# Performance work log

Measured on AMD Instinct MI355X. Metric: run time of the kernel, lower is better.

## Reference

```python
import jax, jax.numpy as jnp
import numpy as np

HEADS = 8
DIM_HEAD = 64
DIM = 512
SCALE = DIM_HEAD ** -0.5
BN_EPS = 1e-5


def setup_inputs() -> dict:
    key = jax.random.key(0)
    ks = jax.random.split(key, 5)
    b, p = 8, 2048
    init = 0.05
    return {
        "x": jax.random.normal(ks[0], (b, p, DIM), jnp.float32),
        "wq": jax.random.normal(ks[1], (HEADS, DIM_HEAD, DIM // HEADS), jnp.float32) * init,
        "wk": jax.random.normal(ks[2], (HEADS, DIM_HEAD, DIM // HEADS), jnp.float32) * init,
        "wv": jax.random.normal(ks[3], (HEADS, DIM_HEAD, DIM // HEADS), jnp.float32) * init,
        "wo": jax.random.normal(ks[4], (DIM, HEADS * DIM_HEAD), jnp.float32) * init,
        "gamma": jnp.ones((DIM,), jnp.float32),
        "beta": jnp.zeros((DIM,), jnp.float32),
    }


def reference(x, wq, wk, wv, wo, gamma, beta):
    # x: [b, p, d]
    b, p, d = x.shape
    h, e = HEADS, DIM_HEAD
    # grouped 1x1 conv == per-head linear on the head's channel slice
    xg = x.reshape(b, p, h, d // h)            # [b, p, h, c]
    q = jnp.einsum('bphc,hec->bhpe', xg, wq)   # [b, h, p, e]
    k = jnp.einsum('bphc,hec->bhpe', xg, wk)
    v = jnp.einsum('bphc,hec->bhpe', xg, wv)
    dots = jnp.einsum('bhie,bhje->bhij', q, k) * SCALE
    attn = jax.nn.softmax(dots, axis=-1)
    out = jnp.einsum('bhij,bhje->bhie', attn, v)     # [b, h, p, e]
    out = out.transpose(0, 2, 1, 3).reshape(b, p, h * e)  # [b, p, inner]
    out = jnp.einsum('bpi,di->bpd', out, wo)         # output 1x1 conv, no bias
    # BatchNorm1d (training mode): stats over (batch, points) per channel
    mean = out.mean(axis=(0, 1))
    var = out.var(axis=(0, 1))
    out = (out - mean) * jax.lax.rsqrt(var + BN_EPS) * gamma + beta
    return jax.nn.relu(out)                          # [b, p, d]
```

## Files before the change

kernel.cpp:

```cpp
#include <hip/hip_runtime.h>
#include <hip/hip_bf16.h>

#define B_ 8
#define P_ 2048
#define D_ 512
#define H_ 8
#define N_ (B_*P_)

using f32x4  = __attribute__((ext_vector_type(4))) float;
using f32x16 = __attribute__((ext_vector_type(16))) float;
using bf16x8 = __attribute__((ext_vector_type(8))) short;

__device__ __forceinline__ unsigned f2bf2(float lo, float hi){
    unsigned short a = __bfloat16_as_ushort(__float2bfloat16(lo));
    unsigned short b = __bfloat16_as_ushort(__float2bfloat16(hi));
    return (unsigned)a | ((unsigned)b << 16);
}
__device__ __forceinline__ unsigned short f2bfu(float x){
    return __bfloat16_as_ushort(__float2bfloat16(x));
}
__device__ __forceinline__ float bf2f(unsigned short u){
    return __uint_as_float(((unsigned)u) << 16);
}
#define SW(r, cb) ((cb) ^ (((r) & 7) << 4))

__device__ __forceinline__ bf16x8 lds_frag(const unsigned char* base, int row, int colb){
    return *(const bf16x8*)(base + row*128 + SW(row, colb));
}

#if __has_builtin(__builtin_amdgcn_exp2f)
#define EXP2(x) __builtin_amdgcn_exp2f(x)
#else
#define EXP2(x) exp2f(x)
#endif

__device__ __forceinline__ void plane32_swap(unsigned &a, unsigned &b){
#if __has_builtin(__builtin_amdgcn_permlane32_swap)
    auto r = __builtin_amdgcn_permlane32_swap(a, b, false, false);
    a = r[0]; b = r[1];
#else
    asm volatile("s_nop 1\n\tv_permlane32_swap_b32 %0, %1\n\ts_nop 1"
                 : "+v"(a), "+v"(b));
#endif
}

#define QSCALE 0.18033688011112042f

__global__ __launch_bounds__(256) void qkv_proj(
        const float* __restrict__ x,
        const float* __restrict__ wq, const float* __restrict__ wk, const float* __restrict__ wv,
        unsigned short* __restrict__ Q, unsigned short* __restrict__ K, unsigned short* __restrict__ Vt)
{
    __shared__ unsigned char xs[128*128];
    __shared__ unsigned char wsh[3][64*128];
    const int t  = threadIdx.x;
    const int bh = blockIdx.x, b = bh >> 3, h = bh & 7;
    const int p0 = blockIdx.y * 128;

    {
        int r = t >> 1, half = t & 1;
        const float4* src = (const float4*)(x + (size_t)(b*P_ + p0 + r)*D_ + h*64 + half*32);
        #pragma unroll
        for (int ci = 0; ci < 4; ci++){
            float4 a = src[ci*2], c = src[ci*2+1];
            uint4 w;
            w.x = f2bf2(a.x, a.y); w.y = f2bf2(a.z, a.w);
            w.z = f2bf2(c.x, c.y); w.w = f2bf2(c.z, c.w);
            *(uint4*)(xs + r*128 + SW(r, half*64 + ci*16)) = w;
        }
    }
    if (t < 192){
        int m = t >> 6, r = t & 63;
        const float* wp = (m == 0 ? wq : (m == 1 ? wk : wv));
        const float4* src = (const float4*)(wp + (size_t)(h*64 + r)*64);
        float sc = (m == 0) ? QSCALE : 1.0f;
        #pragma unroll
        for (int ci = 0; ci < 8; ci++){
            float4 a = src[ci*2], c = src[ci*2+1];
            a.x*=sc;a.y*=sc;a.z*=sc;a.w*=sc; c.x*=sc;c.y*=sc;c.z*=sc;c.w*=sc;
            uint4 w;
            w.x = f2bf2(a.x, a.y); w.y = f2bf2(a.z, a.w);
            w.z = f2bf2(c.x, c.y); w.w = f2bf2(c.z, c.w);
            *(uint4*)(wsh[m] + r*128 + SW(r, ci*16)) = w;
        }
    }
    __syncthreads();
    const int wid = t >> 6, lane = t & 63, g = lane >> 4, l16 = lane & 15;

    bf16x8 fx[2][2];
    #pragma unroll
    for (int pt = 0; pt < 2; pt++)
        #pragma unroll
        for (int kk = 0; kk < 2; kk++)
            fx[pt][kk] = lds_frag(xs, wid*32 + pt*16 + l16, kk*64 + 16*g);

    #pragma unroll
    for (int m = 0; m < 2; m++){
        unsigned short* dst = (m == 0) ? Q : K;
        #pragma unroll
        for (int et = 0; et < 4; et++){
            bf16x8 fw0 = lds_frag(wsh[m], et*16 + l16, 16*g);
            bf16x8 fw1 = lds_frag(wsh[m], et*16 + l16, 64 + 16*g);
            #pragma unroll
            for (int pt = 0; pt < 2; pt++){
                f32x4 acc = {0.f,0.f,0.f,0.f};
                acc = __builtin_amdgcn_mfma_f32_16x16x32_bf16(fw0, fx[pt][0], acc, 0,0,0);
                acc = __builtin_amdgcn_mfma_f32_16x16x32_bf16(fw1, fx[pt][1], acc, 0,0,0);
                int p  = p0 + wid*32 + pt*16 + l16;
                int e0 = et*16 + 4*g;
                uint2 w2; w2.x = f2bf2(acc[0], acc[1]); w2.y = f2bf2(acc[2], acc[3]);
                *(uint2*)(dst + (size_t)(bh*P_ + p)*64 + e0) = w2;
            }
        }
    }
    #pragma unroll
    for (int et = 0; et < 4; et++){
        bf16x8 fw0 = lds_frag(wsh[2], et*16 + l16, 16*g);
        bf16x8 fw1 = lds_frag(wsh[2], et*16 + l16, 64 + 16*g);
        #pragma unroll
        for (int pt = 0; pt < 2; pt++){
            f32x4 acc = {0.f,0.f,0.f,0.f};
            acc = __builtin_amdgcn_mfma_f32_16x16x32_bf16(fx[pt][0], fw0, acc, 0,0,0);
            acc = __builtin_amdgcn_mfma_f32_16x16x32_bf16(fx[pt][1], fw1, acc, 0,0,0);
            int e  = et*16 + l16;
            int pb = p0 + wid*32 + pt*16 + 4*g;
            uint2 w2; w2.x = f2bf2(acc[0], acc[1]); w2.y = f2bf2(acc[2], acc[3]);
            *(uint2*)(Vt + (size_t)(bh*64 + e)*P_ + pb) = w2;
        }
    }
}

__global__ __launch_bounds__(256, 2) void attn_fwd(
        const unsigned short* __restrict__ Q, const unsigned short* __restrict__ K,
        const unsigned short* __restrict__ Vt, unsigned short* __restrict__ AO)
{
    __shared__ unsigned char kshA[64*128], vshA[64*128];
    __shared__ unsigned char kshB[64*128], vshB[64*128];
    const int t  = threadIdx.x;
    const int id = blockIdx.x;
    const int vix = (id & 7) * 128 + (id >> 3);
    const int bh = vix >> 4, b = bh >> 3, h = bh & 7;
    const int q0 = (vix & 15) * 128;
    const int lane = t & 63, wid = t >> 6, hi = lane >> 5, l32 = lane & 31;

    const int qa = q0 + wid*32 + l32;

    bf16x8 fq[4];
    #pragma unroll
    for (int ec = 0; ec < 4; ec++)
        fq[ec] = *(const bf16x8*)(Q + (size_t)(bh*P_ + qa)*64 + ec*16 + hi*8);

    const int srow = t >> 2, sch = t & 3;
    const unsigned short* kgp = K  + ((size_t)bh*P_ + srow)*64 + sch*16;
    const unsigned short* vgp = Vt + ((size_t)(bh*64 + srow))*P_ + sch*16;
    const int wo0 = srow*128 + SW(srow, sch*32);
    const int wo1 = srow*128 + SW(srow, sch*32 + 16);

    f32x16 aco[2];
    #pragma unroll
    for (int r = 0; r < 16; r++){ aco[0][r] = 0.f; aco[1][r] = 0.f; }
    float sml = 0.f;

    uint4 k0, k1, v0, v1;
    auto load_tile = [&](int tt){
        const unsigned short* kp = kgp + (size_t)tt * 4096;
        const unsigned short* vp = vgp + tt * 64;
        k0 = *(const uint4*)kp;        k1 = *(const uint4*)(kp + 8);
        v0 = *(const uint4*)vp;        v1 = *(const uint4*)(vp + 8);
    };
    auto write_tile = [&](unsigned char* ksh, unsigned char* vsh){
        *(uint4*)(ksh + wo0) = k0;  *(uint4*)(ksh + wo1) = k1;
        *(uint4*)(vsh + wo0) = v0;  *(uint4*)(vsh + wo1) = v1;
    };

    auto compute = [&](const unsigned char* ksh, const unsigned char* vsh){
        __builtin_amdgcn_s_setprio(1);
        #pragma unroll
        for (int kb = 0; kb < 2; kb++){
            bf16x8 fk[4], fv[4];
            #pragma unroll
            for (int ec = 0; ec < 4; ec++)
                fk[ec] = *(const bf16x8*)(ksh + (kb*32 + l32)*128 + SW(l32, ec*32 + hi*16));
            #pragma unroll
            for (int sg = 0; sg < 2; sg++)
                #pragma unroll
                for (int eb = 0; eb < 2; eb++)
                    fv[sg*2 + eb] = *(const bf16x8*)(vsh + (eb*32 + l32)*128 + SW(l32, (kb*2 + sg)*32 + hi*16));

            f32x16 s;
            #pragma unroll
            for (int r = 0; r < 16; r++) s[r] = 0.f;
            #pragma unroll
            for (int ec = 0; ec < 4; ec++)
                s = __builtin_amdgcn_mfma_f32_32x32x16_bf16(fk[ec], fq[ec], s, 0, 0, 0);
            float p[16];
            float rs = 0.f;
            #pragma unroll
            for (int r = 0; r < 16; r++){ p[r] = EXP2(s[r]); rs += p[r]; }
            sml += rs;
            #pragma unroll
            for (int sg = 0; sg < 2; sg++){
                unsigned A0 = f2bf2(p[sg*8+0], p[sg*8+1]);
                unsigned A1 = f2bf2(p[sg*8+2], p[sg*8+3]);
                unsigned A2 = f2bf2(p[sg*8+4], p[sg*8+5]);
                unsigned A3 = f2bf2(p[sg*8+6], p[sg*8+7]);
                plane32_swap(A0, A2);
                plane32_swap(A1, A3);
                union { unsigned u[4]; bf16x8 v; } pfu;
                pfu.u[0] = A0; pfu.u[1] = A1; pfu.u[2] = A2; pfu.u[3] = A3;
                #pragma unroll
                for (int eb = 0; eb < 2; eb++)
                    aco[eb] = __builtin_amdgcn_mfma_f32_32x32x16_bf16(fv[sg*2 + eb], pfu.v, aco[eb], 0, 0, 0);
            }
        }
        __builtin_amdgcn_s_setprio(0);
    };

    load_tile(0);
    write_tile(kshA, vshA);
    __syncthreads();

    #pragma unroll 1
    for (int tt = 0; tt < 32; tt += 2){
        load_tile(tt + 1);
        compute(kshA, vshA);
        write_tile(kshB, vshB);
        __syncthreads();
        if (tt + 2 < 32) load_tile(tt + 2);
        compute(kshB, vshB);
        if (tt + 2 < 32){
            write_tile(kshA, vshA);
            __syncthreads();
        }
    }

    float l = sml + __shfl_xor(sml, 32);
    float inv = 1.f / l;
    unsigned short* aor = AO + (size_t)(b*P_ + qa)*D_ + h*64;
    #pragma unroll
    for (int eb = 0; eb < 2; eb++)
        #pragma unroll
        for (int rq = 0; rq < 4; rq++){
            uint2 w;
            w.x = f2bf2(aco[eb][rq*4+0]*inv, aco[eb][rq*4+1]*inv);
            w.y = f2bf2(aco[eb][rq*4+2]*inv, aco[eb][rq*4+3]*inv);
            *(uint2*)(aor + eb*32 + rq*8 + hi*4) = w;
        }
}

__global__ __launch_bounds__(256) void wo_gemm(
        const unsigned short* __restrict__ AO, const float* __restrict__ wo,
        unsigned short* __restrict__ ao2, float* __restrict__ sums)
{
    __shared__ unsigned char ash[128*128];
    __shared__ unsigned char wsh[64*128];
    __shared__ float red[4][2][64];
    const int t  = threadIdx.x;
    const int d0 = blockIdx.x * 64;
    const int n0 = blockIdx.y * 128;
    const int wid = t >> 6, lane = t & 63, g = lane >> 4, l16 = lane & 15;

    f32x4 acc[2][4];
    #pragma unroll
    for (int mt = 0; mt < 2; mt++)
        #pragma unroll
        for (int dt = 0; dt < 4; dt++) acc[mt][dt] = (f32x4){0.f,0.f,0.f,0.f};

    for (int kc = 0; kc < 8; kc++){
        __syncthreads();
        {
            int r = t >> 1, half = t & 1;
            const uint4* src = (const uint4*)(AO + (size_t)(n0 + r)*D_ + kc*64 + half*32);
            #pragma unroll
            for (int i = 0; i < 4; i++)
                *(uint4*)(ash + r*128 + SW(r, half*64 + i*16)) = src[i];
        }
        if (t < 128){
            int r = t >> 1, half = t & 1;
            const float4* src = (const float4*)(wo + (size_t)(d0 + r)*D_ + kc*64 + half*32);
            #pragma unroll
            for (int ci = 0; ci < 4; ci++){
                float4 a = src[ci*2], c = src[ci*2+1];
                uint4 w;
                w.x = f2bf2(a.x, a.y); w.y = f2bf2(a.z, a.w);
                w.z = f2bf2(c.x, c.y); w.w = f2bf2(c.z, c.w);
                *(uint4*)(wsh + r*128 + SW(r, half*64 + ci*16)) = w;
            }
        }
        __syncthreads();
        #pragma unroll
        for (int kk = 0; kk < 2; kk++){
            bf16x8 fa[2], fw[4];
            #pragma unroll
            for (int mt = 0; mt < 2; mt++) fa[mt] = lds_frag(ash, wid*32 + mt*16 + l16, kk*64 + 16*g);
            #pragma unroll
            for (int dt = 0; dt < 4; dt++) fw[dt] = lds_frag(wsh, dt*16 + l16, kk*64 + 16*g);
            #pragma unroll
            for (int mt = 0; mt < 2; mt++)
                #pragma unroll
                for (int dt = 0; dt < 4; dt++)
                    acc[mt][dt] = __builtin_amdgcn_mfma_f32_16x16x32_bf16(fa[mt], fw[dt], acc[mt][dt], 0,0,0);
        }
    }
    float s1[4] = {0.f,0.f,0.f,0.f}, s2[4] = {0.f,0.f,0.f,0.f};
    #pragma unroll
    for (int mt = 0; mt < 2; mt++)
        #pragma unroll
        for (int dt = 0; dt < 4; dt++){
            int d = d0 + dt*16 + l16;
            #pragma unroll
            for (int r = 0; r < 4; r++){
                float v = acc[mt][dt][r];
                ao2[(size_t)(n0 + wid*32 + mt*16 + 4*g + r)*D_ + d] = f2bfu(v);
                s1[dt] += v; s2[dt] += v*v;
            }
        }
    #pragma unroll
    for (int dt = 0; dt < 4; dt++){
        s1[dt] += __shfl_xor(s1[dt], 16); s1[dt] += __shfl_xor(s1[dt], 32);
        s2[dt] += __shfl_xor(s2[dt], 16); s2[dt] += __shfl_xor(s2[dt], 32);
    }
    if (g == 0){
        #pragma unroll
        for (int dt = 0; dt < 4; dt++){
            red[wid][0][dt*16 + l16] = s1[dt];
            red[wid][1][dt*16 + l16] = s2[dt];
        }
    }
    __syncthreads();
    if (t < 128){
        int which = t >> 6, ch = t & 63;
        float v = red[0][which][ch] + red[1][which][ch] + red[2][which][ch] + red[3][which][ch];
        atomicAdd(&sums[which*D_ + d0 + ch], v);
    }
}

__global__ void bn_zero(float* sums){ sums[threadIdx.x] = 0.f; }

__global__ void bn_stats(const float* __restrict__ sums, const float* __restrict__ gamma,
                         const float* __restrict__ beta, float* __restrict__ coef)
{
    int d = threadIdx.x;
    float mean = sums[d] * (1.f/16384.f);
    float var  = sums[512 + d] * (1.f/16384.f) - mean*mean;
    float sc   = gamma[d] * rsqrtf(var + 1e-5f);
    coef[d]       = sc;
    coef[512 + d] = beta[d] - mean*sc;
}

__global__ __launch_bounds__(256) void bn_apply(const unsigned short* __restrict__ ao2,
                                                float* __restrict__ out, const float* __restrict__ coef)
{
    __shared__ float cs[1024];
    int t = threadIdx.x;
    #pragma unroll
    for (int i = 0; i < 4; i++) cs[t + i*256] = coef[t + i*256];
    __syncthreads();
    const int total = N_ * D_ / 8;
    for (int idx = blockIdx.x*256 + t; idx < total; idx += gridDim.x*256){
        uint4 v = *(const uint4*)(ao2 + (size_t)idx*8);
        int d = (idx & 63) * 8;
        float4 o0, o1;
        o0.x = fmaxf(0.f, bf2f((unsigned short)(v.x      ))*cs[d+0] + cs[512+d+0]);
        o0.y = fmaxf(0.f, bf2f((unsigned short)(v.x >> 16))*cs[d+1] + cs[512+d+1]);
        o0.z = fmaxf(0.f, bf2f((unsigned short)(v.y      ))*cs[d+2] + cs[512+d+2]);
        o0.w = fmaxf(0.f, bf2f((unsigned short)(v.y >> 16))*cs[d+3] + cs[512+d+3]);
        o1.x = fmaxf(0.f, bf2f((unsigned short)(v.z      ))*cs[d+4] + cs[512+d+4]);
        o1.y = fmaxf(0.f, bf2f((unsigned short)(v.z >> 16))*cs[d+5] + cs[512+d+5]);
        o1.z = fmaxf(0.f, bf2f((unsigned short)(v.w      ))*cs[d+6] + cs[512+d+6]);
        o1.w = fmaxf(0.f, bf2f((unsigned short)(v.w >> 16))*cs[d+7] + cs[512+d+7]);
        *(float4*)(out + (size_t)idx*8)     = o0;
        *(float4*)(out + (size_t)idx*8 + 4) = o1;
    }
}

extern "C" void kernel_launch(void* const* d_in, const int* in_sizes, int n_in,
                              void* d_out, int out_size, void* d_ws, size_t ws_size,
                              hipStream_t stream)
{
    const float* x     = (const float*)d_in[0];
    const float* wq    = (const float*)d_in[1];
    const float* wk    = (const float*)d_in[2];
    const float* wv    = (const float*)d_in[3];
    const float* wo    = (const float*)d_in[4];
    const float* gamma = (const float*)d_in[5];
    const float* beta  = (const float*)d_in[6];
    float* out = (float*)d_out;

    unsigned char* ws = (unsigned char*)d_ws;
    unsigned short* Q  = (unsigned short*)(ws);
    unsigned short* K  = (unsigned short*)(ws + (16u<<20));
    unsigned short* Vt = (unsigned short*)(ws + (32u<<20));
    unsigned short* AO = (unsigned short*)(ws + (48u<<20));
    float* sums = (float*)(ws + (64u<<20));
    float* coef = sums + 1024;
    unsigned short* AO2 = Q;

    hipLaunchKernelGGL(bn_zero,  dim3(1),       dim3(1024), 0, stream, sums);
    hipLaunchKernelGGL(qkv_proj, dim3(64, 16),  dim3(256),  0, stream, x, wq, wk, wv, Q, K, Vt);
    hipLaunchKernelGGL(attn_fwd, dim3(1024),    dim3(256),  0, stream, Q, K, Vt, AO);
    hipLaunchKernelGGL(wo_gemm,  dim3(8, 128),  dim3(256),  0, stream, AO, wo, AO2, sums);
    hipLaunchKernelGGL(bn_stats, dim3(1),       dim3(512),  0, stream, sums, gamma, beta, coef);
    hipLaunchKernelGGL(bn_apply, dim3(2048),    dim3(256),  0, stream, AO2, out, coef);
}
```

Before: 170.5 us.

## Software-pipeline attention loop: overlap next tile's QK with current tile's softmax+PV

Restructures the flash-attention inner loop so that the QK^T MFMAs for tile t+1 are issued before the exp/pack and PV MFMAs for tile t, carrying V fragments and score accumulators in registers across iterations. The intent is to let the matrix units run while the exponentials and bf16 packing execute, and to hide LDS load latency. In exchange it raises register pressure (extra score accumulators and eight V fragments held live) and adds prologue and epilogue code, which may reduce occupancy.

```diff
diff --git a/kernel.cpp b/kernel.cpp
--- a/kernel.cpp
+++ b/kernel.cpp
@@ -156,9 +156,9 @@
     const int wo0 = srow*128 + SW(srow, sch*32);
     const int wo1 = srow*128 + SW(srow, sch*32 + 16);
 
-    f32x16 aco[2];
-    #pragma unroll
-    for (int r = 0; r < 16; r++){ aco[0][r] = 0.f; aco[1][r] = 0.f; }
+    f32x16 aco0, aco1;
+    #pragma unroll
+    for (int r = 0; r < 16; r++){ aco0[r] = 0.f; aco1[r] = 0.f; }
     float sml = 0.f;
 
     uint4 k0, k1, v0, v1;
@@ -173,30 +173,38 @@
         *(uint4*)(vsh + wo0) = v0;  *(uint4*)(vsh + wo1) = v1;
     };
 
-    auto compute = [&](const unsigned char* ksh, const unsigned char* vsh){
-        __builtin_amdgcn_s_setprio(1);
+    bf16x8 fvc[8];
+    f32x16 sc0, sc1;
+
+    auto qk_tile = [&](const unsigned char* kp_, f32x16& s0, f32x16& s1){
+        bf16x8 fk[8];
+        #pragma unroll
+        for (int kb = 0; kb < 2; kb++)
+            #pragma unroll
+            for (int ec = 0; ec < 4; ec++)
+                fk[kb*4+ec] = *(const bf16x8*)(kp_ + (kb*32 + l32)*128 + SW(l32, ec*32 + hi*16));
+        #pragma unroll
+        for (int r = 0; r < 16; r++){ s0[r] = 0.f; s1[r] = 0.f; }
+        #pragma unroll
+        for (int ec = 0; ec < 4; ec++) s0 = __builtin_amdgcn_mfma_f32_32x32x16_bf16(fk[ec],   fq[ec], s0, 0,0,0);
+        #pragma unroll
+        for (int ec = 0; ec < 4; ec++) s1 = __builtin_amdgcn_mfma_f32_32x32x16_bf16(fk[4+ec], fq[ec], s1, 0,0,0);
+    };
+    auto carry_v = [&](const unsigned char* vp_){
+        #pragma unroll
+        for (int ks = 0; ks < 4; ks++)
+            #pragma unroll
+            for (int eb = 0; eb < 2; eb++)
+                fvc[ks*2+eb] = *(const bf16x8*)(vp_ + (eb*32 + l32)*128 + SW(l32, ks*32 + hi*16));
+    };
+    auto mk_pfu = [&](bf16x8* pfu){
         #pragma unroll
         for (int kb = 0; kb < 2; kb++){
-            bf16x8 fk[4], fv[4];
-            #pragma unroll
-            for (int ec = 0; ec < 4; ec++)
-                fk[ec] = *(const bf16x8*)(ksh + (kb*32 + l32)*128 + SW(l32, ec*32 + hi*16));
-            #pragma unroll
-            for (int sg = 0; sg < 2; sg++)
-                #pragma unroll
-                for (int eb = 0; eb < 2; eb++)
-                    fv[sg*2 + eb] = *(const bf16x8*)(vsh + (eb*32 + l32)*128 + SW(l32, (kb*2 + sg)*32 + hi*16));
-
-            f32x16 s;
-            #pragma unroll
-            for (int r = 0; r < 16; r++) s[r] = 0.f;
-            #pragma unroll
-            for (int ec = 0; ec < 4; ec++)
-                s = __builtin_amdgcn_mfma_f32_32x32x16_bf16(fk[ec], fq[ec], s, 0, 0, 0);
+            const f32x16& sc = kb ? sc1 : sc0;
             float p[16];
             float rs = 0.f;
             #pragma unroll
-            for (int r = 0; r < 16; r++){ p[r] = EXP2(s[r]); rs += p[r]; }
+            for (int r = 0; r < 16; r++){ p[r] = EXP2(sc[r]); rs += p[r]; }
             sml += rs;
             #pragma unroll
             for (int sg = 0; sg < 2; sg++){
@@ -206,46 +214,79 @@
                 unsigned A3 = f2bf2(p[sg*8+6], p[sg*8+7]);
                 plane32_swap(A0, A2);
                 plane32_swap(A1, A3);
-                union { unsigned u[4]; bf16x8 v; } pfu;
-                pfu.u[0] = A0; pfu.u[1] = A1; pfu.u[2] = A2; pfu.u[3] = A3;
-                #pragma unroll
-                for (int eb = 0; eb < 2; eb++)
-                    aco[eb] = __builtin_amdgcn_mfma_f32_32x32x16_bf16(fv[sg*2 + eb], pfu.v, aco[eb], 0, 0, 0);
+                union { unsigned u[4]; bf16x8 v; } pf;
+                pf.u[0]=A0; pf.u[1]=A1; pf.u[2]=A2; pf.u[3]=A3;
+                pfu[kb*2+sg] = pf.v;
             }
         }
-        __builtin_amdgcn_s_setprio(0);
+    };
+    auto pv_tile = [&](const bf16x8* pfu){
+        #pragma unroll
+        for (int ks = 0; ks < 4; ks++){
+            aco0 = __builtin_amdgcn_mfma_f32_32x32x16_bf16(fvc[ks*2+0], pfu[ks], aco0, 0,0,0);
+            aco1 = __builtin_amdgcn_mfma_f32_32x32x16_bf16(fvc[ks*2+1], pfu[ks], aco1, 0,0,0);
+        }
     };
 
     load_tile(0);
     write_tile(kshA, vshA);
     __syncthreads();
+    load_tile(1);
+    qk_tile(kshA, sc0, sc1);
+    carry_v(vshA);
+    write_tile(kshB, vshB);
+    __syncthreads();
+    load_tile(2);
+
+    const unsigned char *kp = kshB, *vp = vshB;
+    unsigned char *kw = kshA, *vw = vshA;
 
     #pragma unroll 1
-    for (int tt = 0; tt < 32; tt += 2){
-        load_tile(tt + 1);
-        compute(kshA, vshA);
-        write_tile(kshB, vshB);
+    for (int tt = 0; tt < 30; ++tt){
+        __builtin_amdgcn_s_setprio(1);
+        f32x16 sn0, sn1;
+        qk_tile(kp, sn0, sn1);
+        bf16x8 pfu[4];
+        mk_pfu(pfu);
+        pv_tile(pfu);
+        __builtin_amdgcn_s_setprio(0);
+        carry_v(vp);
+        sc0 = sn0; sc1 = sn1;
+        write_tile(kw, vw);
         __syncthreads();
-        if (tt + 2 < 32) load_tile(tt + 2);
-        compute(kshB, vshB);
-        if (tt + 2 < 32){
-            write_tile(kshA, vshA);
-            __syncthreads();
-        }
+        if (tt < 29) load_tile(tt + 3);
+        const unsigned char* tk = kp; kp = kw; kw = (unsigned char*)tk;
+        const unsigned char* tv = vp; vp = vw; vw = (unsigned char*)tv;
+    }
+    {
+        f32x16 sn0, sn1;
+        qk_tile(kp, sn0, sn1);
+        bf16x8 pfu[4];
+        mk_pfu(pfu);
+        pv_tile(pfu);
+        carry_v(vp);
+        sc0 = sn0; sc1 = sn1;
+    }
+    {
+        bf16x8 pfu[4];
+        mk_pfu(pfu);
+        pv_tile(pfu);
     }
 
     float l = sml + __shfl_xor(sml, 32);
     float inv = 1.f / l;
     unsigned short* aor = AO + (size_t)(b*P_ + qa)*D_ + h*64;
     #pragma unroll
-    for (int eb = 0; eb < 2; eb++)
+    for (int eb = 0; eb < 2; eb++){
+        const f32x16& a = eb ? aco1 : aco0;
         #pragma unroll
         for (int rq = 0; rq < 4; rq++){
             uint2 w;
-            w.x = f2bf2(aco[eb][rq*4+0]*inv, aco[eb][rq*4+1]*inv);
-            w.y = f2bf2(aco[eb][rq*4+2]*inv, aco[eb][rq*4+3]*inv);
+            w.x = f2bf2(a[rq*4+0]*inv, a[rq*4+1]*inv);
+            w.y = f2bf2(a[rq*4+2]*inv, a[rq*4+3]*inv);
             *(uint2*)(aor + eb*32 + rq*8 + hi*4) = w;
         }
+    }
 }
 
 __global__ __launch_bounds__(256) void wo_gemm(
```

Measured after the change: 174.5 us. +2.3%, slower.

## Store K/V in MFMA fragment order and load fragments directly from global

Applied to the files above, without the earlier changes.

The QKV projection now writes K and V in a pre-swizzled per-tile fragment layout that matches the attention MFMA operand order. The attention kernel then drops its LDS double buffer and block barriers, and each wave reads its K/V fragments straight from global memory with contiguous 16-byte loads. This removes the LDS staging and __syncthreads. In exchange, each of the four waves in a block now fetches the same K/V data from global/L2 on its own instead of sharing it, and the loads are no longer software-pipelined ahead of compute.

```diff
diff --git a/kernel.cpp b/kernel.cpp
--- a/kernel.cpp
+++ b/kernel.cpp
@@ -46,10 +46,17 @@
 
 #define QSCALE 0.18033688011112042f
 
+__device__ __forceinline__ size_t kf_off(int bh, int tt, int kb, int ec, int hi, int l32){
+    return ((size_t)(bh*32 + tt))*4096 + (size_t)(((((kb*4 + ec)*2 + hi)*32) + l32)*8);
+}
+__device__ __forceinline__ size_t vf_off(int bh, int tt, int ks, int eb, int hi, int l32){
+    return ((size_t)(bh*32 + tt))*4096 + (size_t)(((((ks*2 + eb)*2 + hi)*32) + l32)*8);
+}
+
 __global__ __launch_bounds__(256) void qkv_proj(
         const float* __restrict__ x,
         const float* __restrict__ wq, const float* __restrict__ wk, const float* __restrict__ wv,
-        unsigned short* __restrict__ Q, unsigned short* __restrict__ K, unsigned short* __restrict__ Vt)
+        unsigned short* __restrict__ Q, unsigned short* __restrict__ Kf, unsigned short* __restrict__ Vf)
 {
     __shared__ unsigned char xs[128*128];
     __shared__ unsigned char wsh[3][64*128];
@@ -96,7 +103,6 @@
 
     #pragma unroll
     for (int m = 0; m < 2; m++){
-        unsigned short* dst = (m == 0) ? Q : K;
         #pragma unroll
         for (int et = 0; et < 4; et++){
             bf16x8 fw0 = lds_frag(wsh[m], et*16 + l16, 16*g);
@@ -109,7 +115,12 @@
                 int p  = p0 + wid*32 + pt*16 + l16;
                 int e0 = et*16 + 4*g;
                 uint2 w2; w2.x = f2bf2(acc[0], acc[1]); w2.y = f2bf2(acc[2], acc[3]);
-                *(uint2*)(dst + (size_t)(bh*P_ + p)*64 + e0) = w2;
+                if (m == 0){
+                    *(uint2*)(Q + (size_t)(bh*P_ + p)*64 + e0) = w2;
+                } else {
+                    int tt = p >> 6, kvr = p & 63;
+                    *(uint2*)(Kf + kf_off(bh, tt, kvr >> 5, et, g >> 1, kvr & 31) + 4*(g & 1)) = w2;
+                }
             }
         }
     }
@@ -124,18 +135,17 @@
             acc = __builtin_amdgcn_mfma_f32_16x16x32_bf16(fx[pt][1], fw1, acc, 0,0,0);
             int e  = et*16 + l16;
             int pb = p0 + wid*32 + pt*16 + 4*g;
+            int tt = pb >> 6, kvc = pb & 63;
             uint2 w2; w2.x = f2bf2(acc[0], acc[1]); w2.y = f2bf2(acc[2], acc[3]);
-            *(uint2*)(Vt + (size_t)(bh*64 + e)*P_ + pb) = w2;
+            *(uint2*)(Vf + vf_off(bh, tt, kvc >> 4, e >> 5, (kvc >> 3) & 1, e & 31) + (kvc & 7)) = w2;
         }
     }
 }
 
 __global__ __launch_bounds__(256, 2) void attn_fwd(
-        const unsigned short* __restrict__ Q, const unsigned short* __restrict__ K,
-        const unsigned short* __restrict__ Vt, unsigned short* __restrict__ AO)
-{
-    __shared__ unsigned char kshA[64*128], vshA[64*128];
-    __shared__ unsigned char kshB[64*128], vshB[64*128];
+        const unsigned short* __restrict__ Q, const unsigned short* __restrict__ Kf,
+        const unsigned short* __restrict__ Vf, unsigned short* __restrict__ AO)
+{
     const int t  = threadIdx.x;
     const int id = blockIdx.x;
     const int vix = (id & 7) * 128 + (id >> 3);
@@ -150,49 +160,40 @@
     for (int ec = 0; ec < 4; ec++)
         fq[ec] = *(const bf16x8*)(Q + (size_t)(bh*P_ + qa)*64 + ec*16 + hi*8);
 
-    const int srow = t >> 2, sch = t & 3;
-    const unsigned short* kgp = K  + ((size_t)bh*P_ + srow)*64 + sch*16;
-    const unsigned short* vgp = Vt + ((size_t)(bh*64 + srow))*P_ + sch*16;
-    const int wo0 = srow*128 + SW(srow, sch*32);
-    const int wo1 = srow*128 + SW(srow, sch*32 + 16);
+    const unsigned short* kfp = Kf + kf_off(bh, 0, 0, 0, hi, l32);
+    const unsigned short* vfp = Vf + vf_off(bh, 0, 0, 0, hi, l32);
 
     f32x16 aco[2];
     #pragma unroll
     for (int r = 0; r < 16; r++){ aco[0][r] = 0.f; aco[1][r] = 0.f; }
     float sml = 0.f;
 
-    uint4 k0, k1, v0, v1;
-    auto load_tile = [&](int tt){
-        const unsigned short* kp = kgp + (size_t)tt * 4096;
-        const unsigned short* vp = vgp + tt * 64;
-        k0 = *(const uint4*)kp;        k1 = *(const uint4*)(kp + 8);
-        v0 = *(const uint4*)vp;        v1 = *(const uint4*)(vp + 8);
-    };
-    auto write_tile = [&](unsigned char* ksh, unsigned char* vsh){
-        *(uint4*)(ksh + wo0) = k0;  *(uint4*)(ksh + wo1) = k1;
-        *(uint4*)(vsh + wo0) = v0;  *(uint4*)(vsh + wo1) = v1;
-    };
-
-    auto compute = [&](const unsigned char* ksh, const unsigned char* vsh){
+    #pragma unroll 1
+    for (int tt = 0; tt < 32; tt++){
+        const unsigned short* kp = kfp + (size_t)tt * 4096;
+        const unsigned short* vp = vfp + (size_t)tt * 4096;
+
+        bf16x8 fk[8], fv[8];
+        #pragma unroll
+        for (int kb = 0; kb < 2; kb++)
+            #pragma unroll
+            for (int ec = 0; ec < 4; ec++)
+                fk[kb*4+ec] = *(const bf16x8*)(kp + kb*2048 + ec*512);
+        #pragma unroll
+        for (int ks = 0; ks < 4; ks++)
+            #pragma unroll
+            for (int eb = 0; eb < 2; eb++)
+                fv[ks*2+eb] = *(const bf16x8*)(vp + ks*1024 + eb*512);
+
         __builtin_amdgcn_s_setprio(1);
         #pragma unroll
         for (int kb = 0; kb < 2; kb++){
-            bf16x8 fk[4], fv[4];
+            f32x16 s;
+            #pragma unroll
+            for (int r = 0; r < 16; r++) s[r] = 0.f;
             #pragma unroll
             for (int ec = 0; ec < 4; ec++)
-                fk[ec] = *(const bf16x8*)(ksh + (kb*32 + l32)*128 + SW(l32, ec*32 + hi*16));
-            #pragma unroll
-            for (int sg = 0; sg < 2; sg++)
-                #pragma unroll
-                for (int eb = 0; eb < 2; eb++)
-                    fv[sg*2 + eb] = *(const bf16x8*)(vsh + (eb*32 + l32)*128 + SW(l32, (kb*2 + sg)*32 + hi*16));
-
-            f32x16 s;
-            #pragma unroll
-            for (int r = 0; r < 16; r++) s[r] = 0.f;
-            #pragma unroll
-            for (int ec = 0; ec < 4; ec++)
-                s = __builtin_amdgcn_mfma_f32_32x32x16_bf16(fk[ec], fq[ec], s, 0, 0, 0);
+                s = __builtin_amdgcn_mfma_f32_32x32x16_bf16(fk[kb*4+ec], fq[ec], s, 0, 0, 0);
             float p[16];
             float rs = 0.f;
             #pragma unroll
@@ -208,30 +209,13 @@
                 plane32_swap(A1, A3);
                 union { unsigned u[4]; bf16x8 v; } pfu;
                 pfu.u[0] = A0; pfu.u[1] = A1; pfu.u[2] = A2; pfu.u[3] = A3;
+                const int ks = kb*2 + sg;
                 #pragma unroll
                 for (int eb = 0; eb < 2; eb++)
-                    aco[eb] = __builtin_amdgcn_mfma_f32_32x32x16_bf16(fv[sg*2 + eb], pfu.v, aco[eb], 0, 0, 0);
+                    aco[eb] = __builtin_amdgcn_mfma_f32_32x32x16_bf16(fv[ks*2+eb], pfu.v, aco[eb], 0, 0, 0);
             }
         }
         __builtin_amdgcn_s_setprio(0);
-    };
-
-    load_tile(0);
-    write_tile(kshA, vshA);
-    __syncthreads();
-
-    #pragma unroll 1
-    for (int tt = 0; tt < 32; tt += 2){
-        load_tile(tt + 1);
-        compute(kshA, vshA);
-        write_tile(kshB, vshB);
-        __syncthreads();
-        if (tt + 2 < 32) load_tile(tt + 2);
-        compute(kshB, vshB);
-        if (tt + 2 < 32){
-            write_tile(kshA, vshA);
-            __syncthreads();
-        }
     }
 
     float l = sml + __shfl_xor(sml, 32);
@@ -389,16 +373,16 @@
 
     unsigned char* ws = (unsigned char*)d_ws;
     unsigned short* Q  = (unsigned short*)(ws);
-    unsigned short* K  = (unsigned short*)(ws + (16u<<20));
-    unsigned short* Vt = (unsigned short*)(ws + (32u<<20));
+    unsigned short* Kf = (unsigned short*)(ws + (16u<<20));
+    unsigned short* Vf = (unsigned short*)(ws + (32u<<20));
     unsigned short* AO = (unsigned short*)(ws + (48u<<20));
     float* sums = (float*)(ws + (64u<<20));
     float* coef = sums + 1024;
     unsigned short* AO2 = Q;
 
     hipLaunchKernelGGL(bn_zero,  dim3(1),       dim3(1024), 0, stream, sums);
-    hipLaunchKernelGGL(qkv_proj, dim3(64, 16),  dim3(256),  0, stream, x, wq, wk, wv, Q, K, Vt);
-    hipLaunchKernelGGL(attn_fwd, dim3(1024),    dim3(256),  0, stream, Q, K, Vt, AO);
+    hipLaunchKernelGGL(qkv_proj, dim3(64, 16),  dim3(256),  0, stream, x, wq, wk, wv, Q, Kf, Vf);
+    hipLaunchKernelGGL(attn_fwd, dim3(1024),    dim3(256),  0, stream, Q, Kf, Vf, AO);
     hipLaunchKernelGGL(wo_gemm,  dim3(8, 128),  dim3(256),  0, stream, AO, wo, AO2, sums);
     hipLaunchKernelGGL(bn_stats, dim3(1),       dim3(512),  0, stream, sums, gamma, beta, coef);
     hipLaunchKernelGGL(bn_apply, dim3(2048),    dim3(256),  0, stream, AO2, out, coef);
```

Result: no change. 171.2 us (+0.4%).
